# Performance work log

Measured on AMD Instinct MI355X. Metric: run time of the kernel, lower is better.

The kernel has to match this reference:

```python
import jax, jax.numpy as jnp
import numpy as np

# Module hyperparameters (from init_kwargs)
MANHATTAN_WEIGHTS = jnp.asarray([1.0, 1.0, 2.0], dtype=jnp.float32)  # per-xyz weights
R = 0.4       # density radius
ALPHA = 1.0   # density exponent


def setup_inputs() -> dict:
    key = jax.random.key(0)
    k1, k2 = jax.random.split(key)
    B, N, C = 4, 8192, 16
    points = jax.random.normal(k1, (B, N, 3), dtype=jnp.float32)
    features = jax.random.normal(k2, (B, C, N), dtype=jnp.float32)
    return {"points": points, "features": features, "npoint": 2048}


def reference(points, features, npoint):
    """Density + Manhattan weighted furthest point sampling.

    points:   [B, N, 3] xyz coordinates
    features: [B, C, N] (unused by the sampler, kept for API parity)
    returns:  [B, npoint] int32 sampled indices
    """
    B, N, _ = points.shape
    w = MANHATTAN_WEIGHTS.astype(points.dtype)

    # Per-point density: number of neighbors within Euclidean radius R. [B, N]
    d2 = jnp.sum((points[:, :, None, :] - points[:, None, :, :]) ** 2, axis=-1)  # [B,N,N]
    density = jnp.sum(d2 <= R * R, axis=-1).astype(points.dtype)  # >= 1 (includes self)
    penalty = density ** (-ALPHA)  # low-density points get boosted distance

    def step(carry, _):
        min_dist, cur = carry  # [B,N], [B]
        # coordinates of most recently selected point: [B, 1, 3]
        p = jnp.take_along_axis(points, cur[:, None, None].astype(jnp.int32), axis=1)
        # weighted Manhattan distance of every point to the new sample: [B, N]
        d = jnp.sum(w * jnp.abs(points - p), axis=-1)
        min_dist = jnp.minimum(min_dist, d)
        # fused density-weighted furthest-point criterion
        nxt = jnp.argmax(min_dist * penalty, axis=-1).astype(jnp.int32)
        return (min_dist, nxt), cur

    init = (jnp.full((B, N), 1e10, dtype=points.dtype), jnp.zeros((B,), dtype=jnp.int32))
    _, idx = jax.lax.scan(step, init, None, length=npoint)  # idx: [npoint, B]
    return jnp.transpose(idx)  # [B, npoint]
```

## Files before the change

### kernel.cpp

```cpp
#include <hip/hip_runtime.h>


#define NPTS 8192
#define DENS_BLOCK 256
#define DENS_SPLIT 4
#define FPS_THREADS 512
#define FPS_P 16

typedef float v2f __attribute__((ext_vector_type(2)));


__global__ void dfps_density_partial(const float* __restrict__ pts,
                                     unsigned short* __restrict__ pen4, int N) {
#pragma clang fp contract(off)
    const float R2 = (float)(0.4 * 0.4);
    const int b = blockIdx.y;
    const int z = blockIdx.z;
    const int i = blockIdx.x * blockDim.x + threadIdx.x;
    const float* P = pts + (size_t)b * N * 3;

    const v2f px2 = {P[i * 3 + 0], P[i * 3 + 0]};
    const v2f py2 = {P[i * 3 + 1], P[i * 3 + 1]};
    const v2f pz2 = {P[i * 3 + 2], P[i * 3 + 2]};

    const int j0 = z * (N / DENS_SPLIT);
    const int j1 = j0 + (N / DENS_SPLIT);

    int cnt = 0;
#pragma unroll 4
    for (int j = j0; j < j1; j += 2) {
        v2f qx = {P[3 * j + 0], P[3 * j + 3]};
        v2f qy = {P[3 * j + 1], P[3 * j + 4]};
        v2f qz = {P[3 * j + 2], P[3 * j + 5]};
        v2f dx = px2 - qx;
        v2f dy = py2 - qy;
        v2f dz = pz2 - qz;
        v2f d2 = dx * dx;
        d2 = d2 + dy * dy;
        d2 = d2 + dz * dz;
        cnt += (d2.x <= R2) ? 1 : 0;
        cnt += (d2.y <= R2) ? 1 : 0;
    }
    pen4[(size_t)(z * 4 + b) * N + i] = (unsigned short)cnt;
}


#define DPP_STEP(ctrl, rmask)                                                   \
    {                                                                           \
        unsigned int nlo = (unsigned int)__builtin_amdgcn_update_dpp(           \
            0, (int)klo, (ctrl), (rmask), 0xF, false);                          \
        unsigned int nhi = (unsigned int)__builtin_amdgcn_update_dpp(           \
            0, (int)khi, (ctrl), (rmask), 0xF, false);                          \
        unsigned long long o = ((unsigned long long)nhi << 32) | nlo;           \
        unsigned long long c = ((unsigned long long)khi << 32) | klo;           \
        if (o > c) { klo = nlo; khi = nhi; }                                    \
    }

__global__ void __launch_bounds__(FPS_THREADS, 1)
dfps_fps_kernel(const float* __restrict__ pts,
                const unsigned short* __restrict__ pen4,
                const int* __restrict__ npoint_p,
                int* __restrict__ out, int N) {
#pragma clang fp contract(off)
    const int b = blockIdx.x;
    const int tid = threadIdx.x;
    const int lane = tid & 63;
    const int npoint = *npoint_p;
    const float* Pb = pts + (size_t)b * N * 3;
    const int base = tid * FPS_P;

    __shared__ float4 tab[NPTS];
    __shared__ unsigned long long slot[3];

    float x[FPS_P], y[FPS_P], z[FPS_P], pw[FPS_P], v[FPS_P];
#pragma unroll
    for (int k = 0; k < FPS_P; ++k) {
        int idx = base + k;
        x[k] = Pb[idx * 3 + 0];
        y[k] = Pb[idx * 3 + 1];
        z[k] = Pb[idx * 3 + 2];
        int c01 = (int)pen4[(size_t)(0 * 4 + b) * N + idx] +
                  (int)pen4[(size_t)(1 * 4 + b) * N + idx];
        int c23 = (int)pen4[(size_t)(2 * 4 + b) * N + idx] +
                  (int)pen4[(size_t)(3 * 4 + b) * N + idx];
        pw[k] = 1.0f / (float)(c01 + c23);
        v[k] = 1e10f * pw[k];
        tab[idx] = make_float4(x[k], y[k], z[k], 0.f);
    }
    if (tid == 0) { slot[0] = 0ull; slot[2] = 0ull; }
    __syncthreads();

    int cur = 0;
    float cx = Pb[0], cy = Pb[1], cz = Pb[2];

    for (int t = 0; t < npoint; ++t) {
        if (tid == 0) {
            out[(size_t)b * npoint + t] = cur;
            slot[(t + 1) % 3] = 0ull;
        }

        double m0 = 0.0, m1 = 0.0, m2 = 0.0, m3 = 0.0;
#pragma unroll
        for (int k = 0; k < FPS_P; ++k) {
            float d = fabsf(x[k] - cx) + fabsf(y[k] - cy);
            d = fmaf(2.0f, fabsf(z[k] - cz), d);
            float nv = fminf(v[k], d * pw[k]);
            v[k] = nv;
            unsigned long long kb = __double_as_longlong((double)nv) |
                                    (unsigned long long)(unsigned)(N - 1 - (base + k));
            double kd = __longlong_as_double(kb);
            if ((k & 3) == 0)      m0 = fmax(m0, kd);
            else if ((k & 3) == 1) m1 = fmax(m1, kd);
            else if ((k & 3) == 2) m2 = fmax(m2, kd);
            else                   m3 = fmax(m3, kd);
        }
        double ma = fmax(m0, m1);
        double mb = fmax(m2, m3);
        unsigned long long best = __double_as_longlong(fmax(ma, mb));

        unsigned int klo = (unsigned int)best;
        unsigned int khi = (unsigned int)(best >> 32);
        DPP_STEP(0x111, 0xF)
        DPP_STEP(0x112, 0xF)
        DPP_STEP(0x114, 0xF)
        DPP_STEP(0x118, 0xF)
        DPP_STEP(0x142, 0xA)
        DPP_STEP(0x143, 0xC)

        if (lane == 63) {
            unsigned long long wk = ((unsigned long long)khi << 32) | klo;
            atomicMax(&slot[t % 3], wk);
        }
        __syncthreads();

        unsigned long long bk = slot[t % 3];
        cur = (N - 1) - (int)((unsigned int)bk & (unsigned int)(N - 1));
        float4 c = tab[cur];
        cx = c.x;
        cy = c.y;
        cz = c.z;
    }
}

extern "C" void kernel_launch(void* const* d_in, const int* in_sizes, int n_in,
                              void* d_out, int out_size, void* d_ws, size_t ws_size,
                              hipStream_t stream) {
    const float* points  = (const float*)d_in[0];
    const int*   npoint  = (const int*)d_in[2];
    int* out = (int*)d_out;

    const int B = 4;
    const int N = in_sizes[0] / (B * 3);
    unsigned short* pen4 = (unsigned short*)d_ws;

    dim3 dgrid(N / DENS_BLOCK, B, DENS_SPLIT);
    dfps_density_partial<<<dgrid, DENS_BLOCK, 0, stream>>>(points, pen4, N);

    dfps_fps_kernel<<<B, FPS_THREADS, 0, stream>>>(points, pen4, npoint, out, N);
}
```

Baseline: 2.092 ms.

## Split argmax into float max reduction plus index-resolution pass

```diff
diff --git a/kernel.cpp b/kernel.cpp
--- a/kernel.cpp
+++ b/kernel.cpp
@@ -45,15 +45,11 @@
 }
 
 
-#define DPP_STEP(ctrl, rmask)                                                   \
+#define DPP_MAXF(ctrl, rmask)                                                   \
     {                                                                           \
-        unsigned int nlo = (unsigned int)__builtin_amdgcn_update_dpp(           \
-            0, (int)klo, (ctrl), (rmask), 0xF, false);                          \
-        unsigned int nhi = (unsigned int)__builtin_amdgcn_update_dpp(           \
-            0, (int)khi, (ctrl), (rmask), 0xF, false);                          \
-        unsigned long long o = ((unsigned long long)nhi << 32) | nlo;           \
-        unsigned long long c = ((unsigned long long)khi << 32) | klo;           \
-        if (o > c) { klo = nlo; khi = nhi; }                                    \
+        float o_ = __uint_as_float((unsigned)__builtin_amdgcn_update_dpp(       \
+            0, (int)__float_as_uint(mm), (ctrl), (rmask), 0xF, false));         \
+        mm = fmaxf(mm, o_);                                                     \
     }
 
 __global__ void __launch_bounds__(FPS_THREADS, 1)
@@ -70,7 +66,8 @@
     const int base = tid * FPS_P;
 
     __shared__ float4 tab[NPTS];
-    __shared__ unsigned long long slot[3];
+    __shared__ unsigned int vslot[3];
+    __shared__ unsigned int islot[3];
 
     float x[FPS_P], y[FPS_P], z[FPS_P], pw[FPS_P], v[FPS_P];
 #pragma unroll
@@ -87,7 +84,10 @@
         v[k] = 1e10f * pw[k];
         tab[idx] = make_float4(x[k], y[k], z[k], 0.f);
     }
-    if (tid == 0) { slot[0] = 0ull; slot[2] = 0ull; }
+    if (tid == 0) {
+        vslot[0] = 0u; islot[0] = 0xFFFFFFFFu;
+        vslot[2] = 0u; islot[2] = 0xFFFFFFFFu;
+    }
     __syncthreads();
 
     int cur = 0;
@@ -96,45 +96,49 @@
     for (int t = 0; t < npoint; ++t) {
         if (tid == 0) {
             out[(size_t)b * npoint + t] = cur;
-            slot[(t + 1) % 3] = 0ull;
+            vslot[(t + 1) % 3] = 0u;
+            islot[(t + 1) % 3] = 0xFFFFFFFFu;
         }
 
-        double m0 = 0.0, m1 = 0.0, m2 = 0.0, m3 = 0.0;
+        float m0 = 0.f, m1 = 0.f, m2 = 0.f, m3 = 0.f;
 #pragma unroll
         for (int k = 0; k < FPS_P; ++k) {
             float d = fabsf(x[k] - cx) + fabsf(y[k] - cy);
             d = fmaf(2.0f, fabsf(z[k] - cz), d);
             float nv = fminf(v[k], d * pw[k]);
             v[k] = nv;
-            unsigned long long kb = __double_as_longlong((double)nv) |
-                                    (unsigned long long)(unsigned)(N - 1 - (base + k));
-            double kd = __longlong_as_double(kb);
-            if ((k & 3) == 0)      m0 = fmax(m0, kd);
-            else if ((k & 3) == 1) m1 = fmax(m1, kd);
-            else if ((k & 3) == 2) m2 = fmax(m2, kd);
-            else                   m3 = fmax(m3, kd);
+            if ((k & 3) == 0)      m0 = fmaxf(m0, nv);
+            else if ((k & 3) == 1) m1 = fmaxf(m1, nv);
+            else if ((k & 3) == 2) m2 = fmaxf(m2, nv);
+            else                   m3 = fmaxf(m3, nv);
         }
-        double ma = fmax(m0, m1);
-        double mb = fmax(m2, m3);
-        unsigned long long best = __double_as_longlong(fmax(ma, mb));
+        const float tb = fmaxf(fmaxf(m0, m1), fmaxf(m2, m3));
 
-        unsigned int klo = (unsigned int)best;
-        unsigned int khi = (unsigned int)(best >> 32);
-        DPP_STEP(0x111, 0xF)
-        DPP_STEP(0x112, 0xF)
-        DPP_STEP(0x114, 0xF)
-        DPP_STEP(0x118, 0xF)
-        DPP_STEP(0x142, 0xA)
-        DPP_STEP(0x143, 0xC)
+        float mm = tb;
+        DPP_MAXF(0x111, 0xF)
+        DPP_MAXF(0x112, 0xF)
+        DPP_MAXF(0x114, 0xF)
+        DPP_MAXF(0x118, 0xF)
+        DPP_MAXF(0x142, 0xA)
+        DPP_MAXF(0x143, 0xC)
+        if (lane == 63)
+            atomicMax(&vslot[t % 3], __float_as_uint(mm));
 
-        if (lane == 63) {
-            unsigned long long wk = ((unsigned long long)khi << 32) | klo;
-            atomicMax(&slot[t % 3], wk);
-        }
         __syncthreads();
 
-        unsigned long long bk = slot[t % 3];
-        cur = (N - 1) - (int)((unsigned int)bk & (unsigned int)(N - 1));
+        const float bm = __uint_as_float(vslot[t % 3]);
+
+        if (tb == bm) {
+            unsigned cand = 0xFFFFFFFFu;
+#pragma unroll
+            for (int k = 0; k < FPS_P; ++k)
+                if (v[k] == bm) cand = min(cand, (unsigned)(base + k));
+            atomicMin(&islot[t % 3], cand);
+        }
+
+        __syncthreads();
+
+        cur = (int)islot[t % 3];
         float4 c = tab[cur];
         cx = c.x;
         cy = c.y;
```

Result: faster. 1.933 ms (-7.6%).
